# Performance work log

Measured on AMD Instinct MI355X. Metric: run time of the kernel, lower is better.

## Reference

```python
import jax, jax.numpy as jnp
import numpy as np

B = 16384          # graphs (batch)
MAX_NODES = 20     # max nodes per graph
D = 64             # node_embed_dim
DM = 128           # d_model
H = 8              # num_heads
DH = DM // H       # depth per head
SD = 64            # state_embed_dim
N = B * MAX_NODES  # total node rows


def setup_inputs() -> dict:
    key = jax.random.key(0)
    ks = jax.random.split(key, 10)
    node_embed = jax.random.normal(ks[0], (N, D), jnp.float32)
    start_idx = jax.random.randint(ks[1], (B,), 0, N)
    end_idx = jax.random.randint(ks[2], (B,), 0, N)
    # graph id of each node row (agg_state_param = per-graph sum)
    seg_ids = jnp.arange(N, dtype=jnp.int32) // MAX_NODES
    # slots are padding (sparse matmul yields zero rows there) -> idx = -1
    valid = jax.random.uniform(ks[3], (N,)) > 0.2
    pad_idx = jnp.where(valid, jnp.arange(N, dtype=jnp.int32), -1)
    s = 0.05
    Wq = jax.random.normal(ks[4], (3 * D, DM), jnp.float32) * s
    Wk = jax.random.normal(ks[5], (D, DM), jnp.float32) * s
    Wv = jax.random.normal(ks[6], (D, DM), jnp.float32) * s
    Wo = jax.random.normal(ks[7], (DM, SD), jnp.float32) * s
    bq = jnp.zeros((DM,), jnp.float32)
    bk = jnp.zeros((DM,), jnp.float32)
    bv = jnp.zeros((DM,), jnp.float32)
    bo = jnp.zeros((SD,), jnp.float32)
    return {"node_embed": node_embed, "start_idx": start_idx, "end_idx": end_idx,
            "seg_ids": seg_ids, "pad_idx": pad_idx,
            "Wq": Wq, "bq": bq, "Wk": Wk, "bk": bk,
            "Wv": Wv, "bv": bv, "Wo": Wo, "bo": bo}


def reference(node_embed, start_idx, end_idx, seg_ids, pad_idx,
              Wq, bq, Wk, bk, Wv, bv, Wo, bo):
    # sparse one-hot selections -> gathers
    start = node_embed[start_idx]                                  # [B, D]
    end = node_embed[end_idx]                                      # [B, D]
    # agg_state_param -> per-graph sum (segment reduce)
    agg = jax.ops.segment_sum(node_embed, seg_ids, num_segments=B)  # [B, D]
    raw = jnp.concatenate([agg, start, end], axis=1)               # [B, 3D]
    # dropout is identity at inference (training=False)

    # pad_node_param -> gather with zero rows for padded slots
    ok = (pad_idx >= 0)
    nodes = jnp.where(ok[:, None],
                      node_embed[jnp.clip(pad_idx, 0)], 0.0)
    nodes = nodes.reshape(B, MAX_NODES, D)                          # [B, M, D]

    # create_padding_mask: rows whose embedding sums to 0 are padding
    mask = (jnp.sum(nodes, -1) == 0).astype(nodes.dtype)            # [B, M]
    mask = mask[:, None, None, :]                                   # [B,1,1,M]

    q = (raw @ Wq + bq).reshape(B, H, 1, DH)                        # [B,H,1,dh]
    k = (nodes @ Wk + bk).reshape(B, MAX_NODES, H, DH).transpose(0, 2, 1, 3)
    v = (nodes @ Wv + bv).reshape(B, MAX_NODES, H, DH).transpose(0, 2, 1, 3)

    scale = 1.0 / jnp.sqrt(jnp.float32(DH))
    scores = jnp.einsum('bhqd,bhkd->bhqk', q, k) * scale + mask * (-1e9)
    attn = jax.nn.softmax(scores, axis=-1)                          # [B,H,1,M]
    ctx = jnp.einsum('bhqk,bhkd->bhqd', attn, v)                    # [B,H,1,dh]
    ctx = ctx.transpose(0, 2, 1, 3).reshape(B, DM)                  # [B, DM]
    return ctx @ Wo + bo                                            # [B, SD]
```

## Files before the change

kernel.cpp:

```cpp
#include <hip/hip_runtime.h>

#define MAXN 20
#define DD 64
#define DM 128
#define NH 8
#define DH 16
#define SD 64
#define NB 4
#define NROW (NB*MAXN)
#define QKPAD 68

typedef float f32x4 __attribute__((ext_vector_type(4)));
typedef float f32x2 __attribute__((ext_vector_type(2)));

__global__ __launch_bounds__(256) void mha_state_encoder(
    const float* __restrict__ node_embed,
    const int*   __restrict__ start_idx,
    const int*   __restrict__ end_idx,
    const int*   __restrict__ pad_idx,
    const float* __restrict__ Wq, const float* __restrict__ bq,
    const float* __restrict__ Wk, const float* __restrict__ bk,
    const float* __restrict__ Wv, const float* __restrict__ bv,
    const float* __restrict__ Wo, const float* __restrict__ bo,
    float* __restrict__ out)
{
    const int b0 = blockIdx.x * NB;
    const int t  = threadIdx.x;

    __shared__ __align__(16) float nodes[NROW * DD];
    __shared__ __align__(16) float pool[32 * QKPAD];
    __shared__ __align__(16) float pool2[768];
    __shared__ float validf[NROW];

    const float* nbase = node_embed + (size_t)b0 * (MAXN * DD);

    {
        int v = t;
        #pragma unroll
        for (int k2 = 0; k2 < 5; k2++, v += 256) {
            const int row = v >> 4, q = v & 15;
            *(f32x4*)&nodes[(row << 6) + ((q ^ (row & 15)) << 2)] =
                *(const f32x4*)&nbase[(row << 6) + (q << 2)];
        }
    }
    if (t < NROW) validf[t] = (pad_idx[b0 * MAXN + t] >= 0) ? 1.0f : 0.0f;
    {
        const int bb = t >> 6, c = t & 63;
        const float* pg = nbase + bb * (MAXN * DD) + c;
        float s = 0.0f;
        for (int n = 0; n < MAXN; n++) s += pg[n * DD];
        pool2[bb * 192 + c] = s;
        const int rs = start_idx[b0 + bb], re = end_idx[b0 + bb];
        pool2[bb * 192 + DD + c]     = node_embed[(size_t)rs * DD + c];
        pool2[bb * 192 + 2 * DD + c] = node_embed[(size_t)re * DD + c];
    }
    __syncthreads();

    {
        const int jj = (t & 63) * 2;
        const int sg = t >> 6;
        const int i0 = sg * 48;
        f32x2 a0 = {0.f, 0.f}, a1 = a0, a2 = a0, a3 = a0;
        for (int c = 0; c < 12; c++) {
            const int ib = i0 + c * 4;
            const f32x4 r0 = *(const f32x4*)&pool2[0 * 192 + ib];
            const f32x4 r1 = *(const f32x4*)&pool2[1 * 192 + ib];
            const f32x4 r2 = *(const f32x4*)&pool2[2 * 192 + ib];
            const f32x4 r3 = *(const f32x4*)&pool2[3 * 192 + ib];
            #pragma unroll
            for (int u = 0; u < 4; u++) {
                const f32x2 wv = *(const f32x2*)&Wq[(ib + u) * DM + jj];
                a0 += wv * r0[u];
                a1 += wv * r1[u];
                a2 += wv * r2[u];
                a3 += wv * r3[u];
            }
        }
        *(f32x2*)&pool[(sg * NB + 0) * DM + jj] = a0;
        *(f32x2*)&pool[(sg * NB + 1) * DM + jj] = a1;
        *(f32x2*)&pool[(sg * NB + 2) * DM + jj] = a2;
        *(f32x2*)&pool[(sg * NB + 3) * DM + jj] = a3;
    }
    __syncthreads();

    {
        const int bb = t >> 6, c2 = (t & 63) * 2;
        f32x2 s = *(const f32x2*)&bq[c2];
        #pragma unroll
        for (int sg = 0; sg < 4; sg++)
            s += *(const f32x2*)&pool[(sg * NB + bb) * DM + c2];
        *(f32x2*)&pool2[bb * DM + c2] = s;
    }
    __syncthreads();

    #pragma unroll
    for (int pr = 0; pr < 2; pr++) {
        const int pp = t + pr * 256;
        const int h = pp >> 6, i = pp & 63;
        const float* wr = &Wk[i * DM + h * DH];
        const f32x4 w0 = *(const f32x4*)&wr[0];
        const f32x4 w1 = *(const f32x4*)&wr[4];
        const f32x4 w2 = *(const f32x4*)&wr[8];
        const f32x4 w3 = *(const f32x4*)&wr[12];
        #pragma unroll
        for (int bb = 0; bb < NB; bb++) {
            const float* qh = &pool2[bb * DM + h * DH];
            const f32x4 q0 = *(const f32x4*)&qh[0];
            const f32x4 q1 = *(const f32x4*)&qh[4];
            const f32x4 q2 = *(const f32x4*)&qh[8];
            const f32x4 q3 = *(const f32x4*)&qh[12];
            const float s =
                  w0[0]*q0[0] + w0[1]*q0[1] + w0[2]*q0[2] + w0[3]*q0[3]
                + w1[0]*q1[0] + w1[1]*q1[1] + w1[2]*q1[2] + w1[3]*q1[3]
                + w2[0]*q2[0] + w2[1]*q2[1] + w2[2]*q2[2] + w2[3]*q2[3]
                + w3[0]*q3[0] + w3[1]*q3[1] + w3[2]*q3[2] + w3[3]*q3[3];
            pool[(bb * NH + h) * QKPAD + i] = s;
        }
    }
    if (t < NB * NH) {
        const int bb = t >> 3, h = t & 7;
        const float* qh  = &pool2[bb * DM + h * DH];
        const float* bkh = &bk[h * DH];
        float s = 0.0f;
        #pragma unroll
        for (int d = 0; d < DH; d++) s += qh[d] * bkh[d];
        pool2[640 + t] = s;
    }
    __syncthreads();

    {
        const int g = t >> 3;
        const int lane8 = t & 7;
        const int bb = g >> 3;
        const float qbv = pool2[640 + g];
        const int qoff = g * QKPAD;
        const int r0 = bb * MAXN + lane8;
        const int r1 = r0 + 8;
        const int r2 = bb * MAXN + 16 + (lane8 & 3);
        const int B0 = r0 << 6, R0 = r0 & 15;
        const int B1 = r1 << 6, R1 = r1 & 15;
        const int B2 = r2 << 6, R2 = r2 & 15;

        f32x4 A0 = {0.f, 0.f, 0.f, 0.f}, A1 = A0, A2 = A0;
        #pragma unroll
        for (int c = 0; c < 16; c++) {
            const f32x4 qk4 = *(const f32x4*)&pool[qoff + c * 4];
            A0 += qk4 * *(const f32x4*)&nodes[B0 + ((c ^ R0) << 2)];
            A1 += qk4 * *(const f32x4*)&nodes[B1 + ((c ^ R1) << 2)];
            A2 += qk4 * *(const f32x4*)&nodes[B2 + ((c ^ R2) << 2)];
        }
        float v0 = (A0[0] + A0[1] + A0[2] + A0[3] + qbv) * 0.25f;
        float v1 = (A1[0] + A1[1] + A1[2] + A1[3] + qbv) * 0.25f;
        float v2 = (A2[0] + A2[1] + A2[2] + A2[3] + qbv) * 0.25f;
        if (validf[r0] == 0.0f) v0 -= 1.0e9f;
        if (validf[r1] == 0.0f) v1 -= 1.0e9f;
        if (validf[r2] == 0.0f) v2 -= 1.0e9f;

        const float v2m = (lane8 < 4) ? v2 : -3.0e38f;
        float m = fmaxf(fmaxf(v0, v1), v2m);
        m = fmaxf(m, __shfl_xor(m, 1, 8));
        m = fmaxf(m, __shfl_xor(m, 2, 8));
        m = fmaxf(m, __shfl_xor(m, 4, 8));
        const float e0 = __expf(v0 - m);
        const float e1 = __expf(v1 - m);
        const float e2 = (lane8 < 4) ? __expf(v2 - m) : 0.0f;
        float sum = e0 + e1 + e2;
        sum += __shfl_xor(sum, 1, 8);
        sum += __shfl_xor(sum, 2, 8);
        sum += __shfl_xor(sum, 4, 8);
        const float inv = 1.0f / sum;
        pool2[g * MAXN + lane8]     = e0 * inv;
        pool2[g * MAXN + 8 + lane8] = e1 * inv;
        if (lane8 < 4) pool2[g * MAXN + 16 + lane8] = e2 * inv;

        f32x4 acc0 = {0.f, 0.f, 0.f, 0.f}, acc1 = acc0;
        for (int n = 0; n < MAXN; n++) {
            const float a = pool2[g * MAXN + n];
            const int row = bb * MAXN + n;
            const int base = row << 6, R = row & 15;
            acc0 += a * *(const f32x4*)&nodes[base + (((2 * lane8)     ^ R) << 2)];
            acc1 += a * *(const f32x4*)&nodes[base + (((2 * lane8 + 1) ^ R) << 2)];
        }
        *(f32x4*)&pool[g * QKPAD + lane8 * 8]     = acc0;
        *(f32x4*)&pool[g * QKPAD + lane8 * 8 + 4] = acc1;
    }
    __syncthreads();

    {
        const int j = t & 127, bbp = t >> 7;
        const int h = j >> 4;
        const int po0 = ( bbp      * NH + h) * QKPAD;
        const int po1 = ((bbp + 2) * NH + h) * QKPAD;
        float a0 = bv[j], a1 = a0;
        for (int ic = 0; ic < 16; ic++) {
            const f32x4 p0 = *(const f32x4*)&pool[po0 + ic * 4];
            const f32x4 p1 = *(const f32x4*)&pool[po1 + ic * 4];
            #pragma unroll
            for (int u = 0; u < 4; u++) {
                const float wv = Wv[(ic * 4 + u) * DM + j];
                a0 += wv * p0[u];
                a1 += wv * p1[u];
            }
        }
        pool2[ bbp      * DM + j] = a0;
        pool2[(bbp + 2) * DM + j] = a1;
    }
    __syncthreads();

    {
        const int j = t & 63, sg = t >> 6;
        const int i0 = sg * 32;
        float a0 = 0.f, a1 = 0.f, a2 = 0.f, a3 = 0.f;
        for (int ic = 0; ic < 8; ic++) {
            const f32x4 c0 = *(const f32x4*)&pool2[0 * DM + i0 + ic * 4];
            const f32x4 c1 = *(const f32x4*)&pool2[1 * DM + i0 + ic * 4];
            const f32x4 c2 = *(const f32x4*)&pool2[2 * DM + i0 + ic * 4];
            const f32x4 c3 = *(const f32x4*)&pool2[3 * DM + i0 + ic * 4];
            #pragma unroll
            for (int u = 0; u < 4; u++) {
                const float wo = Wo[(i0 + ic * 4 + u) * SD + j];
                a0 += wo * c0[u];
                a1 += wo * c1[u];
                a2 += wo * c2[u];
                a3 += wo * c3[u];
            }
        }
        pool[(sg * NB + 0) * SD + j] = a0;
        pool[(sg * NB + 1) * SD + j] = a1;
        pool[(sg * NB + 2) * SD + j] = a2;
        pool[(sg * NB + 3) * SD + j] = a3;
    }
    __syncthreads();

    {
        const int bb = t >> 6, j = t & 63;
        const float s = bo[j]
            + pool[(0 * NB + bb) * SD + j] + pool[(1 * NB + bb) * SD + j]
            + pool[(2 * NB + bb) * SD + j] + pool[(3 * NB + bb) * SD + j];
        out[(size_t)(b0 + bb) * SD + j] = s;
    }
}

extern "C" void kernel_launch(void* const* d_in, const int* in_sizes, int n_in,
                              void* d_out, int out_size, void* d_ws, size_t ws_size,
                              hipStream_t stream) {
    const float* node_embed = (const float*)d_in[0];
    const int*   start_idx  = (const int*)d_in[1];
    const int*   end_idx    = (const int*)d_in[2];
    const int*   pad_idx    = (const int*)d_in[4];
    const float* Wq = (const float*)d_in[5];
    const float* bq = (const float*)d_in[6];
    const float* Wk = (const float*)d_in[7];
    const float* bk = (const float*)d_in[8];
    const float* Wv = (const float*)d_in[9];
    const float* bv = (const float*)d_in[10];
    const float* Wo = (const float*)d_in[11];
    const float* bo = (const float*)d_in[12];
    float* out = (float*)d_out;

    mha_state_encoder<<<16384 / NB, 256, 0, stream>>>(
        node_embed, start_idx, end_idx, pad_idx,
        Wq, bq, Wk, bk, Wv, bv, Wo, bo, out);
}
```

Before: 196.8 us.

## Process eight graphs per 512-thread block with padded LDS rows and transposed q layout

```diff
diff --git a/kernel.cpp b/kernel.cpp
--- a/kernel.cpp
+++ b/kernel.cpp
@@ -6,14 +6,16 @@
 #define NH 8
 #define DH 16
 #define SD 64
-#define NB 4
+#define NB 8
+#define NT 512
 #define NROW (NB*MAXN)
-#define QKPAD 68
+#define NPAD 68
+#define QKP 68
 
 typedef float f32x4 __attribute__((ext_vector_type(4)));
 typedef float f32x2 __attribute__((ext_vector_type(2)));
 
-__global__ __launch_bounds__(256) void mha_state_encoder(
+__global__ __launch_bounds__(NT) void mha_state_encoder(
     const float* __restrict__ node_embed,
     const int*   __restrict__ start_idx,
     const int*   __restrict__ end_idx,
@@ -27,127 +29,121 @@
     const int b0 = blockIdx.x * NB;
     const int t  = threadIdx.x;
 
-    __shared__ __align__(16) float nodes[NROW * DD];
-    __shared__ __align__(16) float pool[32 * QKPAD];
-    __shared__ __align__(16) float pool2[768];
+    __shared__ __align__(16) float nodes[NROW * NPAD];
+    __shared__ __align__(16) float pool[4608];
+    __shared__ __align__(16) float pool2[1536];
+    __shared__ float qb[NB * NH];
     __shared__ float validf[NROW];
 
     const float* nbase = node_embed + (size_t)b0 * (MAXN * DD);
 
-    {
-        int v = t;
-        #pragma unroll
-        for (int k2 = 0; k2 < 5; k2++, v += 256) {
-            const int row = v >> 4, q = v & 15;
-            *(f32x4*)&nodes[(row << 6) + ((q ^ (row & 15)) << 2)] =
-                *(const f32x4*)&nbase[(row << 6) + (q << 2)];
-        }
-    }
     if (t < NROW) validf[t] = (pad_idx[b0 * MAXN + t] >= 0) ? 1.0f : 0.0f;
     {
-        const int bb = t >> 6, c = t & 63;
+        const int bb = t & 7, c = t >> 3;
         const float* pg = nbase + bb * (MAXN * DD) + c;
         float s = 0.0f;
+        #pragma unroll
         for (int n = 0; n < MAXN; n++) s += pg[n * DD];
-        pool2[bb * 192 + c] = s;
+        pool2[c * 8 + bb] = s;
         const int rs = start_idx[b0 + bb], re = end_idx[b0 + bb];
-        pool2[bb * 192 + DD + c]     = node_embed[(size_t)rs * DD + c];
-        pool2[bb * 192 + 2 * DD + c] = node_embed[(size_t)re * DD + c];
-    }
-    __syncthreads();
-
-    {
-        const int jj = (t & 63) * 2;
-        const int sg = t >> 6;
+        pool2[(DD + c) * 8 + bb]     = node_embed[(size_t)rs * DD + c];
+        pool2[(2 * DD + c) * 8 + bb] = node_embed[(size_t)re * DD + c];
+    }
+    {
+        int v = t;
+        #pragma unroll
+        for (int k = 0; k < 5; k++, v += NT) {
+            const int row = v >> 4, q = (v & 15) * 4;
+            *(f32x4*)&nodes[row * NPAD + q] = *(const f32x4*)&nbase[row * DD + q];
+        }
+    }
+    __syncthreads();
+
+    {
+        const int jp = t & 63;
+        const int bp = (t >> 6) & 1;
+        const int sg = t >> 7;
         const int i0 = sg * 48;
-        f32x2 a0 = {0.f, 0.f}, a1 = a0, a2 = a0, a3 = a0;
-        for (int c = 0; c < 12; c++) {
-            const int ib = i0 + c * 4;
-            const f32x4 r0 = *(const f32x4*)&pool2[0 * 192 + ib];
-            const f32x4 r1 = *(const f32x4*)&pool2[1 * 192 + ib];
-            const f32x4 r2 = *(const f32x4*)&pool2[2 * 192 + ib];
-            const f32x4 r3 = *(const f32x4*)&pool2[3 * 192 + ib];
+        const int c0 = jp * 2;
+        f32x4 aA = {0.f, 0.f, 0.f, 0.f}, aB = aA;
+        for (int i = 0; i < 48; i++) {
+            const f32x2 wv = *(const f32x2*)&Wq[(i0 + i) * DM + c0];
+            const f32x4 r  = *(const f32x4*)&pool2[(i0 + i) * 8 + bp * 4];
+            aA += r * wv[0];
+            aB += r * wv[1];
+        }
+        const int base = sg * 1152 + c0 * 9 + bp * 4;
+        pool[base + 0] = aA[0]; pool[base + 1] = aA[1];
+        pool[base + 2] = aA[2]; pool[base + 3] = aA[3];
+        pool[base + 9] = aB[0]; pool[base + 10] = aB[1];
+        pool[base + 11] = aB[2]; pool[base + 12] = aB[3];
+    }
+    __syncthreads();
+
+    #pragma unroll
+    for (int rep = 0; rep < 2; rep++) {
+        const int v = t + rep * NT;
+        const int bb = v & 7, c = v >> 3;
+        float s = bq[c];
+        #pragma unroll
+        for (int sg = 0; sg < 4; sg++) s += pool[sg * 1152 + c * 9 + bb];
+        pool2[c * 8 + bb] = s;
+    }
+    __syncthreads();
+
+    {
+        const int h = t >> 6, i = t & 63;
+        f32x2 a01 = {0.f, 0.f}, a23 = a01, a45 = a01, a67 = a01;
+        #pragma unroll
+        for (int dq = 0; dq < 4; dq++) {
+            const f32x4 w = *(const f32x4*)&Wk[i * DM + h * DH + dq * 4];
             #pragma unroll
             for (int u = 0; u < 4; u++) {
-                const f32x2 wv = *(const f32x2*)&Wq[(ib + u) * DM + jj];
-                a0 += wv * r0[u];
-                a1 += wv * r1[u];
-                a2 += wv * r2[u];
-                a3 += wv * r3[u];
+                const int d = dq * 4 + u;
+                const f32x4 qa = *(const f32x4*)&pool2[(h * DH + d) * 8];
+                const f32x4 qc = *(const f32x4*)&pool2[(h * DH + d) * 8 + 4];
+                const f32x2 wk2 = {w[u], w[u]};
+                const f32x2 p01 = {qa[0], qa[1]}, p23 = {qa[2], qa[3]};
+                const f32x2 p45 = {qc[0], qc[1]}, p67 = {qc[2], qc[3]};
+                a01 += wk2 * p01; a23 += wk2 * p23;
+                a45 += wk2 * p45; a67 += wk2 * p67;
             }
         }
-        *(f32x2*)&pool[(sg * NB + 0) * DM + jj] = a0;
-        *(f32x2*)&pool[(sg * NB + 1) * DM + jj] = a1;
-        *(f32x2*)&pool[(sg * NB + 2) * DM + jj] = a2;
-        *(f32x2*)&pool[(sg * NB + 3) * DM + jj] = a3;
-    }
-    __syncthreads();
-
-    {
-        const int bb = t >> 6, c2 = (t & 63) * 2;
-        f32x2 s = *(const f32x2*)&bq[c2];
-        #pragma unroll
-        for (int sg = 0; sg < 4; sg++)
-            s += *(const f32x2*)&pool[(sg * NB + bb) * DM + c2];
-        *(f32x2*)&pool2[bb * DM + c2] = s;
-    }
-    __syncthreads();
-
-    #pragma unroll
-    for (int pr = 0; pr < 2; pr++) {
-        const int pp = t + pr * 256;
-        const int h = pp >> 6, i = pp & 63;
-        const float* wr = &Wk[i * DM + h * DH];
-        const f32x4 w0 = *(const f32x4*)&wr[0];
-        const f32x4 w1 = *(const f32x4*)&wr[4];
-        const f32x4 w2 = *(const f32x4*)&wr[8];
-        const f32x4 w3 = *(const f32x4*)&wr[12];
-        #pragma unroll
-        for (int bb = 0; bb < NB; bb++) {
-            const float* qh = &pool2[bb * DM + h * DH];
-            const f32x4 q0 = *(const f32x4*)&qh[0];
-            const f32x4 q1 = *(const f32x4*)&qh[4];
-            const f32x4 q2 = *(const f32x4*)&qh[8];
-            const f32x4 q3 = *(const f32x4*)&qh[12];
-            const float s =
-                  w0[0]*q0[0] + w0[1]*q0[1] + w0[2]*q0[2] + w0[3]*q0[3]
-                + w1[0]*q1[0] + w1[1]*q1[1] + w1[2]*q1[2] + w1[3]*q1[3]
-                + w2[0]*q2[0] + w2[1]*q2[1] + w2[2]*q2[2] + w2[3]*q2[3]
-                + w3[0]*q3[0] + w3[1]*q3[1] + w3[2]*q3[2] + w3[3]*q3[3];
-            pool[(bb * NH + h) * QKPAD + i] = s;
-        }
+        pool[(0 * 8 + h) * QKP + i] = a01[0];
+        pool[(1 * 8 + h) * QKP + i] = a01[1];
+        pool[(2 * 8 + h) * QKP + i] = a23[0];
+        pool[(3 * 8 + h) * QKP + i] = a23[1];
+        pool[(4 * 8 + h) * QKP + i] = a45[0];
+        pool[(5 * 8 + h) * QKP + i] = a45[1];
+        pool[(6 * 8 + h) * QKP + i] = a67[0];
+        pool[(7 * 8 + h) * QKP + i] = a67[1];
     }
     if (t < NB * NH) {
         const int bb = t >> 3, h = t & 7;
-        const float* qh  = &pool2[bb * DM + h * DH];
-        const float* bkh = &bk[h * DH];
         float s = 0.0f;
         #pragma unroll
-        for (int d = 0; d < DH; d++) s += qh[d] * bkh[d];
-        pool2[640 + t] = s;
+        for (int d = 0; d < DH; d++)
+            s += pool2[(h * DH + d) * 8 + bb] * bk[h * DH + d];
+        qb[t] = s;
     }
     __syncthreads();
 
     {
         const int g = t >> 3;
         const int lane8 = t & 7;
-        const int bb = g >> 3;
-        const float qbv = pool2[640 + g];
-        const int qoff = g * QKPAD;
+        const int bb = t >> 6;
+        const float qbv = qb[g];
+        const int qkoff = g * QKP;
         const int r0 = bb * MAXN + lane8;
         const int r1 = r0 + 8;
         const int r2 = bb * MAXN + 16 + (lane8 & 3);
-        const int B0 = r0 << 6, R0 = r0 & 15;
-        const int B1 = r1 << 6, R1 = r1 & 15;
-        const int B2 = r2 << 6, R2 = r2 & 15;
-
         f32x4 A0 = {0.f, 0.f, 0.f, 0.f}, A1 = A0, A2 = A0;
         #pragma unroll
         for (int c = 0; c < 16; c++) {
-            const f32x4 qk4 = *(const f32x4*)&pool[qoff + c * 4];
-            A0 += qk4 * *(const f32x4*)&nodes[B0 + ((c ^ R0) << 2)];
-            A1 += qk4 * *(const f32x4*)&nodes[B1 + ((c ^ R1) << 2)];
-            A2 += qk4 * *(const f32x4*)&nodes[B2 + ((c ^ R2) << 2)];
+            const f32x4 qk4 = *(const f32x4*)&pool[qkoff + c * 4];
+            A0 += qk4 * *(const f32x4*)&nodes[r0 * NPAD + c * 4];
+            A1 += qk4 * *(const f32x4*)&nodes[r1 * NPAD + c * 4];
+            A2 += qk4 * *(const f32x4*)&nodes[r2 * NPAD + c * 4];
         }
         float v0 = (A0[0] + A0[1] + A0[2] + A0[3] + qbv) * 0.25f;
         float v1 = (A1[0] + A1[1] + A1[2] + A1[3] + qbv) * 0.25f;
@@ -176,67 +172,64 @@
         f32x4 acc0 = {0.f, 0.f, 0.f, 0.f}, acc1 = acc0;
         for (int n = 0; n < MAXN; n++) {
             const float a = pool2[g * MAXN + n];
-            const int row = bb * MAXN + n;
-            const int base = row << 6, R = row & 15;
-            acc0 += a * *(const f32x4*)&nodes[base + (((2 * lane8)     ^ R) << 2)];
-            acc1 += a * *(const f32x4*)&nodes[base + (((2 * lane8 + 1) ^ R) << 2)];
-        }
-        *(f32x4*)&pool[g * QKPAD + lane8 * 8]     = acc0;
-        *(f32x4*)&pool[g * QKPAD + lane8 * 8 + 4] = acc1;
-    }
-    __syncthreads();
-
-    {
-        const int j = t & 127, bbp = t >> 7;
-        const int h = j >> 4;
-        const int po0 = ( bbp      * NH + h) * QKPAD;
-        const int po1 = ((bbp + 2) * NH + h) * QKPAD;
-        float a0 = bv[j], a1 = a0;
+            const float* nr = &nodes[(bb * MAXN + n) * NPAD + lane8 * 8];
+            acc0 += a * *(const f32x4*)nr;
+            acc1 += a * *(const f32x4*)(nr + 4);
+        }
+        *(f32x4*)&pool[g * QKP + lane8 * 8]     = acc0;
+        *(f32x4*)&pool[g * QKP + lane8 * 8 + 4] = acc1;
+    }
+    __syncthreads();
+
+    {
+        const int jp = t & 63, bb = t >> 6;
+        const int c0 = jp * 2, h = jp >> 3;
+        const int poff = (bb * 8 + h) * QKP;
+        f32x2 a = {bv[c0], bv[c0 + 1]};
+        #pragma unroll
         for (int ic = 0; ic < 16; ic++) {
-            const f32x4 p0 = *(const f32x4*)&pool[po0 + ic * 4];
-            const f32x4 p1 = *(const f32x4*)&pool[po1 + ic * 4];
+            const f32x4 p4 = *(const f32x4*)&pool[poff + ic * 4];
             #pragma unroll
             for (int u = 0; u < 4; u++) {
-                const float wv = Wv[(ic * 4 + u) * DM + j];
-                a0 += wv * p0[u];
-                a1 += wv * p1[u];
+                const f32x2 wv = *(const f32x2*)&Wv[(ic * 4 + u) * DM + c0];
+                a += wv * p4[u];
             }
         }
-        pool2[ bbp      * DM + j] = a0;
-        pool2[(bbp + 2) * DM + j] = a1;
+        *(f32x2*)&pool2[bb * DM + c0] = a;
     }
     __syncthreads();
 
     {
         const int j = t & 63, sg = t >> 6;
-        const int i0 = sg * 32;
-        float a0 = 0.f, a1 = 0.f, a2 = 0.f, a3 = 0.f;
-        for (int ic = 0; ic < 8; ic++) {
-            const f32x4 c0 = *(const f32x4*)&pool2[0 * DM + i0 + ic * 4];
-            const f32x4 c1 = *(const f32x4*)&pool2[1 * DM + i0 + ic * 4];
-            const f32x4 c2 = *(const f32x4*)&pool2[2 * DM + i0 + ic * 4];
-            const f32x4 c3 = *(const f32x4*)&pool2[3 * DM + i0 + ic * 4];
-            #pragma unroll
-            for (int u = 0; u < 4; u++) {
-                const float wo = Wo[(i0 + ic * 4 + u) * SD + j];
-                a0 += wo * c0[u];
-                a1 += wo * c1[u];
-                a2 += wo * c2[u];
-                a3 += wo * c3[u];
-            }
-        }
-        pool[(sg * NB + 0) * SD + j] = a0;
-        pool[(sg * NB + 1) * SD + j] = a1;
-        pool[(sg * NB + 2) * SD + j] = a2;
-        pool[(sg * NB + 3) * SD + j] = a3;
+        const int i0 = sg * 16;
+        f32x2 a01 = {0.f, 0.f}, a23 = a01, a45 = a01, a67 = a01;
+        for (int i = 0; i < 16; i++) {
+            const int ii = i0 + i;
+            const float wo = Wo[ii * SD + j];
+            const f32x2 w2 = {wo, wo};
+            const f32x2 c01 = {pool2[0 * DM + ii], pool2[1 * DM + ii]};
+            const f32x2 c23 = {pool2[2 * DM + ii], pool2[3 * DM + ii]};
+            const f32x2 c45 = {pool2[4 * DM + ii], pool2[5 * DM + ii]};
+            const f32x2 c67 = {pool2[6 * DM + ii], pool2[7 * DM + ii]};
+            a01 += w2 * c01; a23 += w2 * c23;
+            a45 += w2 * c45; a67 += w2 * c67;
+        }
+        pool[sg * 512 + 0 * SD + j] = a01[0];
+        pool[sg * 512 + 1 * SD + j] = a01[1];
+        pool[sg * 512 + 2 * SD + j] = a23[0];
+        pool[sg * 512 + 3 * SD + j] = a23[1];
+        pool[sg * 512 + 4 * SD + j] = a45[0];
+        pool[sg * 512 + 5 * SD + j] = a45[1];
+        pool[sg * 512 + 6 * SD + j] = a67[0];
+        pool[sg * 512 + 7 * SD + j] = a67[1];
     }
     __syncthreads();
 
     {
         const int bb = t >> 6, j = t & 63;
-        const float s = bo[j]
-            + pool[(0 * NB + bb) * SD + j] + pool[(1 * NB + bb) * SD + j]
-            + pool[(2 * NB + bb) * SD + j] + pool[(3 * NB + bb) * SD + j];
+        float s = bo[j];
+        #pragma unroll
+        for (int sg = 0; sg < 8; sg++) s += pool[sg * 512 + bb * SD + j];
         out[(size_t)(b0 + bb) * SD + j] = s;
     }
 }
@@ -258,7 +251,7 @@
     const float* bo = (const float*)d_in[12];
     float* out = (float*)d_out;
 
-    mha_state_encoder<<<16384 / NB, 256, 0, stream>>>(
+    mha_state_encoder<<<16384 / NB, NT, 0, stream>>>(
         node_embed, start_idx, end_idx, pad_idx,
         Wq, bq, Wk, bk, Wv, bv, Wo, bo, out);
 }
```

Result: slower. 223.7 us (+13.7%).

## Give each wavefront one graph after the Q stage and drop block barriers

Applied to the files above, without the earlier changes.

```diff
diff --git a/kernel.cpp b/kernel.cpp
--- a/kernel.cpp
+++ b/kernel.cpp
@@ -8,7 +8,7 @@
 #define SD 64
 #define NB 4
 #define NROW (NB*MAXN)
-#define QKPAD 68
+#define QKP 68
 
 typedef float f32x4 __attribute__((ext_vector_type(4)));
 typedef float f32x2 __attribute__((ext_vector_type(2)));
@@ -28,8 +28,8 @@
     const int t  = threadIdx.x;
 
     __shared__ __align__(16) float nodes[NROW * DD];
-    __shared__ __align__(16) float pool[32 * QKPAD];
-    __shared__ __align__(16) float pool2[768];
+    __shared__ __align__(16) float pool[32 * QKP];
+    __shared__ __align__(16) float pool2[1408];
     __shared__ float validf[NROW];
 
     const float* nbase = node_embed + (size_t)b0 * (MAXN * DD);
@@ -93,47 +93,45 @@
     }
     __syncthreads();
 
-    #pragma unroll
-    for (int pr = 0; pr < 2; pr++) {
-        const int pp = t + pr * 256;
-        const int h = pp >> 6, i = pp & 63;
-        const float* wr = &Wk[i * DM + h * DH];
-        const f32x4 w0 = *(const f32x4*)&wr[0];
-        const f32x4 w1 = *(const f32x4*)&wr[4];
-        const f32x4 w2 = *(const f32x4*)&wr[8];
-        const f32x4 w3 = *(const f32x4*)&wr[12];
-        #pragma unroll
-        for (int bb = 0; bb < NB; bb++) {
-            const float* qh = &pool2[bb * DM + h * DH];
-            const f32x4 q0 = *(const f32x4*)&qh[0];
-            const f32x4 q1 = *(const f32x4*)&qh[4];
-            const f32x4 q2 = *(const f32x4*)&qh[8];
-            const f32x4 q3 = *(const f32x4*)&qh[12];
+    const int w = t >> 6;
+    const int ell = t & 63;
+
+    {
+        const float* qvw = &pool2[w * DM];
+        #pragma unroll
+        for (int h = 0; h < NH; h++) {
+            const f32x4 q0 = *(const f32x4*)&qvw[h * DH + 0];
+            const f32x4 q1 = *(const f32x4*)&qvw[h * DH + 4];
+            const f32x4 q2 = *(const f32x4*)&qvw[h * DH + 8];
+            const f32x4 q3 = *(const f32x4*)&qvw[h * DH + 12];
+            const float* wr = &Wk[ell * DM + h * DH];
+            const f32x4 w0 = *(const f32x4*)&wr[0];
+            const f32x4 w1 = *(const f32x4*)&wr[4];
+            const f32x4 w2 = *(const f32x4*)&wr[8];
+            const f32x4 w3 = *(const f32x4*)&wr[12];
             const float s =
                   w0[0]*q0[0] + w0[1]*q0[1] + w0[2]*q0[2] + w0[3]*q0[3]
                 + w1[0]*q1[0] + w1[1]*q1[1] + w1[2]*q1[2] + w1[3]*q1[3]
                 + w2[0]*q2[0] + w2[1]*q2[1] + w2[2]*q2[2] + w2[3]*q2[3]
                 + w3[0]*q3[0] + w3[1]*q3[1] + w3[2]*q3[2] + w3[3]*q3[3];
-            pool[(bb * NH + h) * QKPAD + i] = s;
-        }
-    }
-    if (t < NB * NH) {
-        const int bb = t >> 3, h = t & 7;
-        const float* qh  = &pool2[bb * DM + h * DH];
-        const float* bkh = &bk[h * DH];
-        float s = 0.0f;
-        #pragma unroll
-        for (int d = 0; d < DH; d++) s += qh[d] * bkh[d];
-        pool2[640 + t] = s;
-    }
-    __syncthreads();
+            pool[(w * NH + h) * QKP + ell] = s;
+        }
+        if (ell < NH) {
+            const float* qh  = &pool2[w * DM + ell * DH];
+            const float* bkh = &bk[ell * DH];
+            float s = 0.0f;
+            #pragma unroll
+            for (int d = 0; d < DH; d++) s += qh[d] * bkh[d];
+            pool2[640 + w * NH + ell] = s;
+        }
+    }
 
     {
         const int g = t >> 3;
         const int lane8 = t & 7;
-        const int bb = g >> 3;
+        const int bb = w;
         const float qbv = pool2[640 + g];
-        const int qoff = g * QKPAD;
+        const int qoff = g * QKP;
         const int r0 = bb * MAXN + lane8;
         const int r1 = r0 + 8;
         const int r2 = bb * MAXN + 16 + (lane8 & 3);
@@ -169,75 +167,54 @@
         sum += __shfl_xor(sum, 2, 8);
         sum += __shfl_xor(sum, 4, 8);
         const float inv = 1.0f / sum;
-        pool2[g * MAXN + lane8]     = e0 * inv;
-        pool2[g * MAXN + 8 + lane8] = e1 * inv;
-        if (lane8 < 4) pool2[g * MAXN + 16 + lane8] = e2 * inv;
+        const int at = 768 + g * MAXN;
+        pool2[at + lane8]     = e0 * inv;
+        pool2[at + 8 + lane8] = e1 * inv;
+        if (lane8 < 4) pool2[at + 16 + lane8] = e2 * inv;
 
         f32x4 acc0 = {0.f, 0.f, 0.f, 0.f}, acc1 = acc0;
         for (int n = 0; n < MAXN; n++) {
-            const float a = pool2[g * MAXN + n];
+            const float a = pool2[at + n];
             const int row = bb * MAXN + n;
             const int base = row << 6, R = row & 15;
             acc0 += a * *(const f32x4*)&nodes[base + (((2 * lane8)     ^ R) << 2)];
             acc1 += a * *(const f32x4*)&nodes[base + (((2 * lane8 + 1) ^ R) << 2)];
         }
-        *(f32x4*)&pool[g * QKPAD + lane8 * 8]     = acc0;
-        *(f32x4*)&pool[g * QKPAD + lane8 * 8 + 4] = acc1;
-    }
-    __syncthreads();
-
-    {
-        const int j = t & 127, bbp = t >> 7;
-        const int h = j >> 4;
-        const int po0 = ( bbp      * NH + h) * QKPAD;
-        const int po1 = ((bbp + 2) * NH + h) * QKPAD;
-        float a0 = bv[j], a1 = a0;
+        *(f32x4*)&pool[g * QKP + lane8 * 8]     = acc0;
+        *(f32x4*)&pool[g * QKP + lane8 * 8 + 4] = acc1;
+    }
+
+    {
+        const int j = ell;
+        const int hA = j >> 4, hB = 4 + (j >> 4);
+        const int pA = (w * NH + hA) * QKP;
+        const int pB = (w * NH + hB) * QKP;
+        float a0 = bv[j], a1 = bv[j + 64];
+        #pragma unroll
         for (int ic = 0; ic < 16; ic++) {
-            const f32x4 p0 = *(const f32x4*)&pool[po0 + ic * 4];
-            const f32x4 p1 = *(const f32x4*)&pool[po1 + ic * 4];
+            const f32x4 p0 = *(const f32x4*)&pool[pA + ic * 4];
+            const f32x4 p1 = *(const f32x4*)&pool[pB + ic * 4];
             #pragma unroll
             for (int u = 0; u < 4; u++) {
-                const float wv = Wv[(ic * 4 + u) * DM + j];
-                a0 += wv * p0[u];
-                a1 += wv * p1[u];
+                a0 += Wv[(ic * 4 + u) * DM + j]      * p0[u];
+                a1 += Wv[(ic * 4 + u) * DM + j + 64] * p1[u];
             }
         }
-        pool2[ bbp      * DM + j] = a0;
-        pool2[(bbp + 2) * DM + j] = a1;
-    }
-    __syncthreads();
-
-    {
-        const int j = t & 63, sg = t >> 6;
-        const int i0 = sg * 32;
-        float a0 = 0.f, a1 = 0.f, a2 = 0.f, a3 = 0.f;
-        for (int ic = 0; ic < 8; ic++) {
-            const f32x4 c0 = *(const f32x4*)&pool2[0 * DM + i0 + ic * 4];
-            const f32x4 c1 = *(const f32x4*)&pool2[1 * DM + i0 + ic * 4];
-            const f32x4 c2 = *(const f32x4*)&pool2[2 * DM + i0 + ic * 4];
-            const f32x4 c3 = *(const f32x4*)&pool2[3 * DM + i0 + ic * 4];
-            #pragma unroll
-            for (int u = 0; u < 4; u++) {
-                const float wo = Wo[(i0 + ic * 4 + u) * SD + j];
-                a0 += wo * c0[u];
-                a1 += wo * c1[u];
-                a2 += wo * c2[u];
-                a3 += wo * c3[u];
-            }
-        }
-        pool[(sg * NB + 0) * SD + j] = a0;
-        pool[(sg * NB + 1) * SD + j] = a1;
-        pool[(sg * NB + 2) * SD + j] = a2;
-        pool[(sg * NB + 3) * SD + j] = a3;
-    }
-    __syncthreads();
-
-    {
-        const int bb = t >> 6, j = t & 63;
-        const float s = bo[j]
-            + pool[(0 * NB + bb) * SD + j] + pool[(1 * NB + bb) * SD + j]
-            + pool[(2 * NB + bb) * SD + j] + pool[(3 * NB + bb) * SD + j];
-        out[(size_t)(b0 + bb) * SD + j] = s;
+        pool2[w * DM + j]      = a0;
+        pool2[w * DM + j + 64] = a1;
+    }
+
+    {
+        const int j = ell;
+        float acc = bo[j];
+        #pragma unroll
+        for (int ic = 0; ic < 32; ic++) {
+            const f32x4 c4 = *(const f32x4*)&pool2[w * DM + ic * 4];
+            #pragma unroll
+            for (int u = 0; u < 4; u++)
+                acc += Wo[(ic * 4 + u) * SD + j] * c4[u];
+        }
+        out[(size_t)(b0 + w) * SD + j] = acc;
     }
 }
 
```

After: 251.8 us. +27.9%, slower.

## Split Q projection into separate MFMA kernel using split-bf16 precision emulation

Applied to the files above, without the earlier changes.

```diff
diff --git a/kernel.cpp b/kernel.cpp
--- a/kernel.cpp
+++ b/kernel.cpp
@@ -8,28 +8,148 @@
 #define SD 64
 #define NB 4
 #define NROW (NB*MAXN)
-#define QKPAD 68
+#define QKP 68
+
+#define ABATCH 32
+#define QV_BYTES (16384ull * DM * 4ull)
+#define BFRAG_BYTES (192 * DM * 2 * 2ull)
 
 typedef float f32x4 __attribute__((ext_vector_type(4)));
 typedef float f32x2 __attribute__((ext_vector_type(2)));
-
-__global__ __launch_bounds__(256) void mha_state_encoder(
+typedef __bf16 bf16x8 __attribute__((ext_vector_type(8)));
+
+__global__ __launch_bounds__(256) void prep_wq(
+    const float* __restrict__ Wq, unsigned short* __restrict__ bfrag)
+{
+    int idx = blockIdx.x * 256 + threadIdx.x;
+    int e  = idx & 7;
+    int l  = (idx >> 3) & 63;
+    int h  = (idx >> 9) & 1;
+    int r  = idx >> 10;
+    int kt = r % 6;
+    int nt = r / 6;
+    int k   = kt * 32 + (l >> 4) * 8 + e;
+    int col = nt * 16 + (l & 15);
+    float w = Wq[k * DM + col];
+    __bf16 hi = (__bf16)w;
+    __bf16 v  = h ? (__bf16)(w - (float)hi) : hi;
+    bfrag[idx] = __builtin_bit_cast(unsigned short, v);
+}
+
+__global__ __launch_bounds__(256) void qproj(
     const float* __restrict__ node_embed,
     const int*   __restrict__ start_idx,
     const int*   __restrict__ end_idx,
+    const float* __restrict__ bq,
+    const unsigned short* __restrict__ bfrag,
+    float* __restrict__ qv_ws)
+{
+    const int b0 = blockIdx.x * ABATCH;
+    const int t  = threadIdx.x;
+    __shared__ __align__(16) float rawq[ABATCH * 192];
+
+    const float* nbase = node_embed + (size_t)b0 * (MAXN * DD);
+
+    #pragma unroll
+    for (int i = 0; i < 8; i++) {
+        const int v = t + i * 256;
+        const int bb = v >> 6, c = v & 63;
+        const float* pg = nbase + bb * (MAXN * DD) + c;
+        float s = 0.0f;
+        #pragma unroll
+        for (int n = 0; n < MAXN; n++) s += pg[n * DD];
+        rawq[bb * 192 + c] = s;
+        const int rs = start_idx[b0 + bb], re = end_idx[b0 + bb];
+        rawq[bb * 192 + DD + c]     = node_embed[(size_t)rs * DD + c];
+        rawq[bb * 192 + 2 * DD + c] = node_embed[(size_t)re * DD + c];
+    }
+    __syncthreads();
+
+    const int w = t >> 6, l = t & 63;
+    const int r15 = l & 15, kg = (l >> 4) * 8;
+    f32x4 a00 = {0.f,0.f,0.f,0.f}, a01 = a00, a10 = a00, a11 = a00;
+    const bf16x8* bf = (const bf16x8*)bfrag;
+
+    for (int kt = 0; kt < 6; kt++) {
+        bf16x8 Ah0, Al0, Ah1, Al1;
+        {
+            const float* p = &rawq[r15 * 192 + kt * 32 + kg];
+            const f32x4 x0 = *(const f32x4*)p;
+            const f32x4 x1 = *(const f32x4*)(p + 4);
+            #pragma unroll
+            for (int e = 0; e < 8; e++) {
+                const float xe = (e < 4) ? x0[e] : x1[e - 4];
+                const __bf16 hi = (__bf16)xe;
+                Ah0[e] = hi; Al0[e] = (__bf16)(xe - (float)hi);
+            }
+            const float* q = &rawq[(16 + r15) * 192 + kt * 32 + kg];
+            const f32x4 y0 = *(const f32x4*)q;
+            const f32x4 y1 = *(const f32x4*)(q + 4);
+            #pragma unroll
+            for (int e = 0; e < 8; e++) {
+                const float xe = (e < 4) ? y0[e] : y1[e - 4];
+                const __bf16 hi = (__bf16)xe;
+                Ah1[e] = hi; Al1[e] = (__bf16)(xe - (float)hi);
+            }
+        }
+        {
+            const int fb = ((w * 6 + kt) * 2) * 64 + l;
+            const bf16x8 Bh = bf[fb], Bl = bf[fb + 64];
+            a00 = __builtin_amdgcn_mfma_f32_16x16x32_bf16(Ah0, Bh, a00, 0, 0, 0);
+            a10 = __builtin_amdgcn_mfma_f32_16x16x32_bf16(Ah1, Bh, a10, 0, 0, 0);
+            a00 = __builtin_amdgcn_mfma_f32_16x16x32_bf16(Al0, Bh, a00, 0, 0, 0);
+            a10 = __builtin_amdgcn_mfma_f32_16x16x32_bf16(Al1, Bh, a10, 0, 0, 0);
+            a00 = __builtin_amdgcn_mfma_f32_16x16x32_bf16(Ah0, Bl, a00, 0, 0, 0);
+            a10 = __builtin_amdgcn_mfma_f32_16x16x32_bf16(Ah1, Bl, a10, 0, 0, 0);
+        }
+        {
+            const int fb = (((w + 4) * 6 + kt) * 2) * 64 + l;
+            const bf16x8 Bh = bf[fb], Bl = bf[fb + 64];
+            a01 = __builtin_amdgcn_mfma_f32_16x16x32_bf16(Ah0, Bh, a01, 0, 0, 0);
+            a11 = __builtin_amdgcn_mfma_f32_16x16x32_bf16(Ah1, Bh, a11, 0, 0, 0);
+            a01 = __builtin_amdgcn_mfma_f32_16x16x32_bf16(Al0, Bh, a01, 0, 0, 0);
+            a11 = __builtin_amdgcn_mfma_f32_16x16x32_bf16(Al1, Bh, a11, 0, 0, 0);
+            a01 = __builtin_amdgcn_mfma_f32_16x16x32_bf16(Ah0, Bl, a01, 0, 0, 0);
+            a11 = __builtin_amdgcn_mfma_f32_16x16x32_bf16(Ah1, Bl, a11, 0, 0, 0);
+        }
+    }
+    const int rb = (l >> 4) * 4;
+    {
+        const int col = w * 16 + r15;
+        const float bqc = bq[col];
+        #pragma unroll
+        for (int r = 0; r < 4; r++) {
+            qv_ws[(size_t)(b0 + rb + r) * DM + col]      = a00[r] + bqc;
+            qv_ws[(size_t)(b0 + 16 + rb + r) * DM + col] = a10[r] + bqc;
+        }
+    }
+    {
+        const int col = (w + 4) * 16 + r15;
+        const float bqc = bq[col];
+        #pragma unroll
+        for (int r = 0; r < 4; r++) {
+            qv_ws[(size_t)(b0 + rb + r) * DM + col]      = a01[r] + bqc;
+            qv_ws[(size_t)(b0 + 16 + rb + r) * DM + col] = a11[r] + bqc;
+        }
+    }
+}
+
+__global__ __launch_bounds__(256) void mha_attn(
+    const float* __restrict__ node_embed,
     const int*   __restrict__ pad_idx,
-    const float* __restrict__ Wq, const float* __restrict__ bq,
-    const float* __restrict__ Wk, const float* __restrict__ bk,
+    const float* __restrict__ bk,
+    const float* __restrict__ Wk,
     const float* __restrict__ Wv, const float* __restrict__ bv,
     const float* __restrict__ Wo, const float* __restrict__ bo,
+    const float* __restrict__ qv_ws,
     float* __restrict__ out)
 {
     const int b0 = blockIdx.x * NB;
     const int t  = threadIdx.x;
 
     __shared__ __align__(16) float nodes[NROW * DD];
-    __shared__ __align__(16) float pool[32 * QKPAD];
-    __shared__ __align__(16) float pool2[768];
+    __shared__ __align__(16) float pool[32 * QKP];
+    __shared__ __align__(16) float pool2[832];
     __shared__ float validf[NROW];
 
     const float* nbase = node_embed + (size_t)b0 * (MAXN * DD);
@@ -44,53 +164,7 @@
         }
     }
     if (t < NROW) validf[t] = (pad_idx[b0 * MAXN + t] >= 0) ? 1.0f : 0.0f;
-    {
-        const int bb = t >> 6, c = t & 63;
-        const float* pg = nbase + bb * (MAXN * DD) + c;
-        float s = 0.0f;
-        for (int n = 0; n < MAXN; n++) s += pg[n * DD];
-        pool2[bb * 192 + c] = s;
-        const int rs = start_idx[b0 + bb], re = end_idx[b0 + bb];
-        pool2[bb * 192 + DD + c]     = node_embed[(size_t)rs * DD + c];
-        pool2[bb * 192 + 2 * DD + c] = node_embed[(size_t)re * DD + c];
-    }
-    __syncthreads();
-
-    {
-        const int jj = (t & 63) * 2;
-        const int sg = t >> 6;
-        const int i0 = sg * 48;
-        f32x2 a0 = {0.f, 0.f}, a1 = a0, a2 = a0, a3 = a0;
-        for (int c = 0; c < 12; c++) {
-            const int ib = i0 + c * 4;
-            const f32x4 r0 = *(const f32x4*)&pool2[0 * 192 + ib];
-            const f32x4 r1 = *(const f32x4*)&pool2[1 * 192 + ib];
-            const f32x4 r2 = *(const f32x4*)&pool2[2 * 192 + ib];
-            const f32x4 r3 = *(const f32x4*)&pool2[3 * 192 + ib];
-            #pragma unroll
-            for (int u = 0; u < 4; u++) {
-                const f32x2 wv = *(const f32x2*)&Wq[(ib + u) * DM + jj];
-                a0 += wv * r0[u];
-                a1 += wv * r1[u];
-                a2 += wv * r2[u];
-                a3 += wv * r3[u];
-            }
-        }
-        *(f32x2*)&pool[(sg * NB + 0) * DM + jj] = a0;
-        *(f32x2*)&pool[(sg * NB + 1) * DM + jj] = a1;
-        *(f32x2*)&pool[(sg * NB + 2) * DM + jj] = a2;
-        *(f32x2*)&pool[(sg * NB + 3) * DM + jj] = a3;
-    }
-    __syncthreads();
-
-    {
-        const int bb = t >> 6, c2 = (t & 63) * 2;
-        f32x2 s = *(const f32x2*)&bq[c2];
-        #pragma unroll
-        for (int sg = 0; sg < 4; sg++)
-            s += *(const f32x2*)&pool[(sg * NB + bb) * DM + c2];
-        *(f32x2*)&pool2[bb * DM + c2] = s;
-    }
+    *(f32x2*)&pool2[t * 2] = *(const f32x2*)&qv_ws[(size_t)b0 * DM + t * 2];
     __syncthreads();
 
     #pragma unroll
@@ -114,7 +188,7 @@
                 + w1[0]*q1[0] + w1[1]*q1[1] + w1[2]*q1[2] + w1[3]*q1[3]
                 + w2[0]*q2[0] + w2[1]*q2[1] + w2[2]*q2[2] + w2[3]*q2[3]
                 + w3[0]*q3[0] + w3[1]*q3[1] + w3[2]*q3[2] + w3[3]*q3[3];
-            pool[(bb * NH + h) * QKPAD + i] = s;
+            pool[(bb * NH + h) * QKP + i] = s;
         }
     }
     if (t < NB * NH) {
@@ -124,7 +198,7 @@
         float s = 0.0f;
         #pragma unroll
         for (int d = 0; d < DH; d++) s += qh[d] * bkh[d];
-        pool2[640 + t] = s;
+        pool2[768 + t] = s;
     }
     __syncthreads();
 
@@ -132,8 +206,8 @@
         const int g = t >> 3;
         const int lane8 = t & 7;
         const int bb = g >> 3;
-        const float qbv = pool2[640 + g];
-        const int qoff = g * QKPAD;
+        const float qbv = pool2[768 + g];
+        const int qoff = g * QKP;
         const int r0 = bb * MAXN + lane8;
         const int r1 = r0 + 8;
         const int r2 = bb * MAXN + 16 + (lane8 & 3);
@@ -181,16 +255,16 @@
             acc0 += a * *(const f32x4*)&nodes[base + (((2 * lane8)     ^ R) << 2)];
             acc1 += a * *(const f32x4*)&nodes[base + (((2 * lane8 + 1) ^ R) << 2)];
         }
-        *(f32x4*)&pool[g * QKPAD + lane8 * 8]     = acc0;
-        *(f32x4*)&pool[g * QKPAD + lane8 * 8 + 4] = acc1;
+        *(f32x4*)&pool[g * QKP + lane8 * 8]     = acc0;
+        *(f32x4*)&pool[g * QKP + lane8 * 8 + 4] = acc1;
     }
     __syncthreads();
 
     {
         const int j = t & 127, bbp = t >> 7;
         const int h = j >> 4;
-        const int po0 = ( bbp      * NH + h) * QKPAD;
-        const int po1 = ((bbp + 2) * NH + h) * QKPAD;
+        const int po0 = ( bbp      * NH + h) * QKP;
+        const int po1 = ((bbp + 2) * NH + h) * QKP;
         float a0 = bv[j], a1 = a0;
         for (int ic = 0; ic < 16; ic++) {
             const f32x4 p0 = *(const f32x4*)&pool[po0 + ic * 4];
@@ -232,6 +306,217 @@
     }
     __syncthreads();
 
+    {
+        const int bb = t >> 6, j = t & 63;
+        const float s = bo[j]
+            + pool[(0 * NB + bb) * SD + j] + pool[(1 * NB + bb) * SD + j]
+            + pool[(2 * NB + bb) * SD + j] + pool[(3 * NB + bb) * SD + j];
+        out[(size_t)(b0 + bb) * SD + j] = s;
+    }
+}
+
+__global__ __launch_bounds__(256) void mha_r7(
+    const float* __restrict__ node_embed,
+    const int*   __restrict__ start_idx,
+    const int*   __restrict__ end_idx,
+    const int*   __restrict__ pad_idx,
+    const float* __restrict__ Wq, const float* __restrict__ bq,
+    const float* __restrict__ Wk, const float* __restrict__ bk,
+    const float* __restrict__ Wv, const float* __restrict__ bv,
+    const float* __restrict__ Wo, const float* __restrict__ bo,
+    float* __restrict__ out)
+{
+    const int b0 = blockIdx.x * NB;
+    const int t  = threadIdx.x;
+    __shared__ __align__(16) float nodes[NROW * DD];
+    __shared__ __align__(16) float pool[32 * QKP];
+    __shared__ __align__(16) float pool2[768];
+    __shared__ float validf[NROW];
+    const float* nbase = node_embed + (size_t)b0 * (MAXN * DD);
+    {
+        int v = t;
+        #pragma unroll
+        for (int k2 = 0; k2 < 5; k2++, v += 256) {
+            const int row = v >> 4, q = v & 15;
+            *(f32x4*)&nodes[(row << 6) + ((q ^ (row & 15)) << 2)] =
+                *(const f32x4*)&nbase[(row << 6) + (q << 2)];
+        }
+    }
+    if (t < NROW) validf[t] = (pad_idx[b0 * MAXN + t] >= 0) ? 1.0f : 0.0f;
+    {
+        const int bb = t >> 6, c = t & 63;
+        const float* pg = nbase + bb * (MAXN * DD) + c;
+        float s = 0.0f;
+        for (int n = 0; n < MAXN; n++) s += pg[n * DD];
+        pool2[bb * 192 + c] = s;
+        const int rs = start_idx[b0 + bb], re = end_idx[b0 + bb];
+        pool2[bb * 192 + DD + c]     = node_embed[(size_t)rs * DD + c];
+        pool2[bb * 192 + 2 * DD + c] = node_embed[(size_t)re * DD + c];
+    }
+    __syncthreads();
+    {
+        const int jj = (t & 63) * 2;
+        const int sg = t >> 6;
+        const int i0 = sg * 48;
+        f32x2 a0 = {0.f, 0.f}, a1 = a0, a2 = a0, a3 = a0;
+        for (int c = 0; c < 12; c++) {
+            const int ib = i0 + c * 4;
+            const f32x4 r0 = *(const f32x4*)&pool2[0 * 192 + ib];
+            const f32x4 r1 = *(const f32x4*)&pool2[1 * 192 + ib];
+            const f32x4 r2 = *(const f32x4*)&pool2[2 * 192 + ib];
+            const f32x4 r3 = *(const f32x4*)&pool2[3 * 192 + ib];
+            #pragma unroll
+            for (int u = 0; u < 4; u++) {
+                const f32x2 wv = *(const f32x2*)&Wq[(ib + u) * DM + jj];
+                a0 += wv * r0[u]; a1 += wv * r1[u];
+                a2 += wv * r2[u]; a3 += wv * r3[u];
+            }
+        }
+        *(f32x2*)&pool[(sg * NB + 0) * DM + jj] = a0;
+        *(f32x2*)&pool[(sg * NB + 1) * DM + jj] = a1;
+        *(f32x2*)&pool[(sg * NB + 2) * DM + jj] = a2;
+        *(f32x2*)&pool[(sg * NB + 3) * DM + jj] = a3;
+    }
+    __syncthreads();
+    {
+        const int bb = t >> 6, c2 = (t & 63) * 2;
+        f32x2 s = *(const f32x2*)&bq[c2];
+        #pragma unroll
+        for (int sg = 0; sg < 4; sg++)
+            s += *(const f32x2*)&pool[(sg * NB + bb) * DM + c2];
+        *(f32x2*)&pool2[bb * DM + c2] = s;
+    }
+    __syncthreads();
+    #pragma unroll
+    for (int pr = 0; pr < 2; pr++) {
+        const int pp = t + pr * 256;
+        const int h = pp >> 6, i = pp & 63;
+        const float* wr = &Wk[i * DM + h * DH];
+        const f32x4 w0 = *(const f32x4*)&wr[0];
+        const f32x4 w1 = *(const f32x4*)&wr[4];
+        const f32x4 w2 = *(const f32x4*)&wr[8];
+        const f32x4 w3 = *(const f32x4*)&wr[12];
+        #pragma unroll
+        for (int bb = 0; bb < NB; bb++) {
+            const float* qh = &pool2[bb * DM + h * DH];
+            const f32x4 q0 = *(const f32x4*)&qh[0];
+            const f32x4 q1 = *(const f32x4*)&qh[4];
+            const f32x4 q2 = *(const f32x4*)&qh[8];
+            const f32x4 q3 = *(const f32x4*)&qh[12];
+            const float s =
+                  w0[0]*q0[0] + w0[1]*q0[1] + w0[2]*q0[2] + w0[3]*q0[3]
+                + w1[0]*q1[0] + w1[1]*q1[1] + w1[2]*q1[2] + w1[3]*q1[3]
+                + w2[0]*q2[0] + w2[1]*q2[1] + w2[2]*q2[2] + w2[3]*q2[3]
+                + w3[0]*q3[0] + w3[1]*q3[1] + w3[2]*q3[2] + w3[3]*q3[3];
+            pool[(bb * NH + h) * QKP + i] = s;
+        }
+    }
+    if (t < NB * NH) {
+        const int bb = t >> 3, h = t & 7;
+        const float* qh  = &pool2[bb * DM + h * DH];
+        const float* bkh = &bk[h * DH];
+        float s = 0.0f;
+        #pragma unroll
+        for (int d = 0; d < DH; d++) s += qh[d] * bkh[d];
+        pool2[640 + t] = s;
+    }
+    __syncthreads();
+    {
+        const int g = t >> 3;
+        const int lane8 = t & 7;
+        const int bb = g >> 3;
+        const float qbv = pool2[640 + g];
+        const int qoff = g * QKP;
+        const int r0 = bb * MAXN + lane8;
+        const int r1 = r0 + 8;
+        const int r2 = bb * MAXN + 16 + (lane8 & 3);
+        const int B0 = r0 << 6, R0 = r0 & 15;
+        const int B1 = r1 << 6, R1 = r1 & 15;
+        const int B2 = r2 << 6, R2 = r2 & 15;
+        f32x4 A0 = {0.f, 0.f, 0.f, 0.f}, A1 = A0, A2 = A0;
+        #pragma unroll
+        for (int c = 0; c < 16; c++) {
+            const f32x4 qk4 = *(const f32x4*)&pool[qoff + c * 4];
+            A0 += qk4 * *(const f32x4*)&nodes[B0 + ((c ^ R0) << 2)];
+            A1 += qk4 * *(const f32x4*)&nodes[B1 + ((c ^ R1) << 2)];
+            A2 += qk4 * *(const f32x4*)&nodes[B2 + ((c ^ R2) << 2)];
+        }
+        float v0 = (A0[0] + A0[1] + A0[2] + A0[3] + qbv) * 0.25f;
+        float v1 = (A1[0] + A1[1] + A1[2] + A1[3] + qbv) * 0.25f;
+        float v2 = (A2[0] + A2[1] + A2[2] + A2[3] + qbv) * 0.25f;
+        if (validf[r0] == 0.0f) v0 -= 1.0e9f;
+        if (validf[r1] == 0.0f) v1 -= 1.0e9f;
+        if (validf[r2] == 0.0f) v2 -= 1.0e9f;
+        const float v2m = (lane8 < 4) ? v2 : -3.0e38f;
+        float m = fmaxf(fmaxf(v0, v1), v2m);
+        m = fmaxf(m, __shfl_xor(m, 1, 8));
+        m = fmaxf(m, __shfl_xor(m, 2, 8));
+        m = fmaxf(m, __shfl_xor(m, 4, 8));
+        const float e0 = __expf(v0 - m);
+        const float e1 = __expf(v1 - m);
+        const float e2 = (lane8 < 4) ? __expf(v2 - m) : 0.0f;
+        float sum = e0 + e1 + e2;
+        sum += __shfl_xor(sum, 1, 8);
+        sum += __shfl_xor(sum, 2, 8);
+        sum += __shfl_xor(sum, 4, 8);
+        const float inv = 1.0f / sum;
+        pool2[g * MAXN + lane8]     = e0 * inv;
+        pool2[g * MAXN + 8 + lane8] = e1 * inv;
+        if (lane8 < 4) pool2[g * MAXN + 16 + lane8] = e2 * inv;
+        f32x4 acc0 = {0.f, 0.f, 0.f, 0.f}, acc1 = acc0;
+        for (int n = 0; n < MAXN; n++) {
+            const float a = pool2[g * MAXN + n];
+            const int row = bb * MAXN + n;
+            const int base = row << 6, R = row & 15;
+            acc0 += a * *(const f32x4*)&nodes[base + (((2 * lane8)     ^ R) << 2)];
+            acc1 += a * *(const f32x4*)&nodes[base + (((2 * lane8 + 1) ^ R) << 2)];
+        }
+        *(f32x4*)&pool[g * QKP + lane8 * 8]     = acc0;
+        *(f32x4*)&pool[g * QKP + lane8 * 8 + 4] = acc1;
+    }
+    __syncthreads();
+    {
+        const int j = t & 127, bbp = t >> 7;
+        const int h = j >> 4;
+        const int po0 = ( bbp      * NH + h) * QKP;
+        const int po1 = ((bbp + 2) * NH + h) * QKP;
+        float a0 = bv[j], a1 = a0;
+        for (int ic = 0; ic < 16; ic++) {
+            const f32x4 p0 = *(const f32x4*)&pool[po0 + ic * 4];
+            const f32x4 p1 = *(const f32x4*)&pool[po1 + ic * 4];
+            #pragma unroll
+            for (int u = 0; u < 4; u++) {
+                const float wv = Wv[(ic * 4 + u) * DM + j];
+                a0 += wv * p0[u];
+                a1 += wv * p1[u];
+            }
+        }
+        pool2[ bbp      * DM + j] = a0;
+        pool2[(bbp + 2) * DM + j] = a1;
+    }
+    __syncthreads();
+    {
+        const int j = t & 63, sg = t >> 6;
+        const int i0 = sg * 32;
+        float a0 = 0.f, a1 = 0.f, a2 = 0.f, a3 = 0.f;
+        for (int ic = 0; ic < 8; ic++) {
+            const f32x4 c0 = *(const f32x4*)&pool2[0 * DM + i0 + ic * 4];
+            const f32x4 c1 = *(const f32x4*)&pool2[1 * DM + i0 + ic * 4];
+            const f32x4 c2 = *(const f32x4*)&pool2[2 * DM + i0 + ic * 4];
+            const f32x4 c3 = *(const f32x4*)&pool2[3 * DM + i0 + ic * 4];
+            #pragma unroll
+            for (int u = 0; u < 4; u++) {
+                const float wo = Wo[(i0 + ic * 4 + u) * SD + j];
+                a0 += wo * c0[u]; a1 += wo * c1[u];
+                a2 += wo * c2[u]; a3 += wo * c3[u];
+            }
+        }
+        pool[(sg * NB + 0) * SD + j] = a0;
+        pool[(sg * NB + 1) * SD + j] = a1;
+        pool[(sg * NB + 2) * SD + j] = a2;
+        pool[(sg * NB + 3) * SD + j] = a3;
+    }
+    __syncthreads();
     {
         const int bb = t >> 6, j = t & 63;
         const float s = bo[j]
@@ -258,7 +543,17 @@
     const float* bo = (const float*)d_in[12];
     float* out = (float*)d_out;
 
-    mha_state_encoder<<<16384 / NB, 256, 0, stream>>>(
-        node_embed, start_idx, end_idx, pad_idx,
-        Wq, bq, Wk, bk, Wv, bv, Wo, bo, out);
+    if (ws_size >= QV_BYTES + BFRAG_BYTES) {
+        float* qv_ws = (float*)d_ws;
+        unsigned short* bfrag = (unsigned short*)((char*)d_ws + QV_BYTES);
+        prep_wq<<<192, 256, 0, stream>>>(Wq, bfrag);
+        qproj<<<16384 / ABATCH, 256, 0, stream>>>(
+            node_embed, start_idx, end_idx, bq, bfrag, qv_ws);
+        mha_attn<<<16384 / NB, 256, 0, stream>>>(
+            node_embed, pad_idx, bk, Wk, Wv, bv, Wo, bo, qv_ws, out);
+    } else {
+        mha_r7<<<16384 / NB, 256, 0, stream>>>(
+            node_embed, start_idx, end_idx, pad_idx,
+            Wq, bq, Wk, bk, Wv, bv, Wo, bo, out);
+    }
 }
```

Result: no change. 197.6 us (+0.4%).
